# Kernel optimization log

Hardware: AMD Instinct MI355X
Metric: run time of the kernel (lower is better)

## Reference

```python
import jax, jax.numpy as jnp
import numpy as np

NUM_EMB = 16384
EMB_DIM = 64
BETA = 0.25  # commitment_cost, legacy=True formulation


def _l2norm(x, axis=-1):
    # matches F.normalize(p=2): x / max(||x||, 1e-12)
    n = jnp.sqrt(jnp.sum(x * x, axis=axis, keepdims=True))
    return x / jnp.maximum(n, 1e-12)


def setup_inputs() -> dict:
    key = jax.random.key(0)
    k_z, k_cb, k_w, k_b = jax.random.split(key, 4)
    z = jax.random.normal(k_z, (16, 1024, EMB_DIM), dtype=jnp.float32)
    # frozen codebook: N(0, d^{-0.5})
    codebook = jax.random.normal(k_cb, (NUM_EMB, EMB_DIM), dtype=jnp.float32) * (EMB_DIM ** -0.5)
    # Linear(d, d) default init: U(-1/sqrt(d), 1/sqrt(d))
    lim = 1.0 / np.sqrt(EMB_DIM)
    proj_w = jax.random.uniform(k_w, (EMB_DIM, EMB_DIM), dtype=jnp.float32, minval=-lim, maxval=lim)
    proj_b = jax.random.uniform(k_b, (EMB_DIM,), dtype=jnp.float32, minval=-lim, maxval=lim)
    scale = jnp.float32(10.0)  # l2_norm_scale
    return {"z": z, "codebook": codebook, "proj_w": proj_w, "proj_b": proj_b, "scale": scale}


def reference(z, codebook, proj_w, proj_b, scale):
    B, T, d = z.shape
    zf = z.reshape(-1, d)                                   # [BT, d]
    quant_codebook = codebook @ proj_w.T + proj_b           # [N, d]
    zn = _l2norm(zf)
    cn = _l2norm(quant_codebook)
    distances = -jnp.einsum('bd,nd->bn', zn, cn) * scale    # [BT, N]
    idx = jnp.argmin(distances, axis=1)                     # [BT]
    quantized = quant_codebook[idx].reshape(z.shape)        # [B, T, d]
    sg = jax.lax.stop_gradient
    commitment_loss = jnp.mean((sg(quantized) - z) ** 2)
    codebook_loss = jnp.mean((quantized - sg(z)) ** 2)
    vq_loss = commitment_loss + BETA * codebook_loss        # legacy=True
    quantized_st = z + sg(quantized - z)                    # straight-through
    return quantized_st, vq_loss, idx.reshape(B, T)
```

## Files before the change

### kernel.cpp

```cpp
#include <hip/hip_runtime.h>
#include <hip/hip_bf16.h>


#define NCODES 16384
#define NTOK   16384
#define DIM    64
#define MARGIN_MFMA 8e-3f
#define CAP    16

typedef __attribute__((ext_vector_type(8))) short bf16x8;
typedef __attribute__((ext_vector_type(4))) float f32x4;
#define GLOBAL_AS __attribute__((address_space(1)))
#define LDS_AS    __attribute__((address_space(3)))

__device__ float  g_qcb[NCODES * DIM];
__device__ short  g_cnb[NCODES * DIM];
__device__ short  g_znb[NTOK * DIM];
__device__ unsigned g_topu[NTOK];
__device__ int    g_candcnt[NTOK];
__device__ int    g_cand[NTOK * CAP];
__device__ int    g_wl[NTOK];
__device__ int    g_wln;
__device__ float  g_partial[512];

__device__ __forceinline__ float wave_sum64(float v) {
#pragma unroll
  for (int o = 32; o > 0; o >>= 1) v += __shfl_xor(v, o, 64);
  return v;
}
__device__ __forceinline__ short f2bf(float f) {
  __hip_bfloat16 h = __float2bfloat16(f);
  return *reinterpret_cast<short*>(&h);
}
__device__ __forceinline__ float bf2f(short s) {
  __hip_bfloat16 h = *reinterpret_cast<__hip_bfloat16*>(&s);
  return __bfloat162float(h);
}
__device__ __forceinline__ void split8(const float* v, bf16x8& hi, bf16x8& lo) {
#pragma unroll
  for (int i = 0; i < 8; ++i) {
    float f = v[i];
    short h = f2bf(f);
    hi[i] = h;
    lo[i] = f2bf(f - bf2f(h));
  }
}

__global__ __launch_bounds__(256) void k_prep(const float* __restrict__ cb,
                                              const float* __restrict__ pw,
                                              const float* __restrict__ pb,
                                              const float* __restrict__ z) {
  int tid = threadIdx.x;
  int wave = tid >> 6, lane = tid & 63, quad = lane >> 4, col = lane & 15;
  if (blockIdx.x < 256) {
    int rowBase = blockIdx.x * 64 + wave * 16;
    const float* cr = cb + (size_t)(rowBase + col) * 64 + quad * 8;
    bf16x8 ah0, al0, ah1, al1;
    split8(cr, ah0, al0);
    split8(cr + 32, ah1, al1);
    float vals[4][4];
    float nr[4] = {0.f, 0.f, 0.f, 0.f};
    const f32x4 fz = {0.f, 0.f, 0.f, 0.f};
#pragma unroll
    for (int nt = 0; nt < 4; ++nt) {
      int j = col + 16 * nt;
      const float* wr = pw + (size_t)j * 64 + quad * 8;
      bf16x8 bh0, bl0, bh1, bl1;
      split8(wr, bh0, bl0);
      split8(wr + 32, bh1, bl1);
      f32x4 d = __builtin_amdgcn_mfma_f32_16x16x32_bf16(ah0, bh0, fz, 0, 0, 0);
      d = __builtin_amdgcn_mfma_f32_16x16x32_bf16(ah1, bh1, d, 0, 0, 0);
      d = __builtin_amdgcn_mfma_f32_16x16x32_bf16(ah0, bl0, d, 0, 0, 0);
      d = __builtin_amdgcn_mfma_f32_16x16x32_bf16(ah1, bl1, d, 0, 0, 0);
      d = __builtin_amdgcn_mfma_f32_16x16x32_bf16(al0, bh0, d, 0, 0, 0);
      d = __builtin_amdgcn_mfma_f32_16x16x32_bf16(al1, bh1, d, 0, 0, 0);
      float bj = pb[j];
#pragma unroll
      for (int r = 0; r < 4; ++r) {
        float v = d[r] + bj;
        vals[nt][r] = v;
        nr[r] = fmaf(v, v, nr[r]);
      }
    }
#pragma unroll
    for (int r = 0; r < 4; ++r) {
      float v = nr[r];
      v += __shfl_xor(v, 1, 64);
      v += __shfl_xor(v, 2, 64);
      v += __shfl_xor(v, 4, 64);
      v += __shfl_xor(v, 8, 64);
      nr[r] = 1.0f / fmaxf(sqrtf(v), 1e-12f);
    }
#pragma unroll
    for (int nt = 0; nt < 4; ++nt)
#pragma unroll
      for (int r = 0; r < 4; ++r) {
        int row = rowBase + quad * 4 + r;
        int j = col + 16 * nt;
        g_qcb[(size_t)row * 64 + j] = vals[nt][r];
        g_cnb[(size_t)row * 64 + j] = f2bf(vals[nt][r] * nr[r]);
      }
  } else {
    int zb = blockIdx.x - 256;
    int gid = zb * 256 + tid;
    if (gid < NTOK) { g_topu[gid] = 0u; g_candcnt[gid] = 0; }
    if (gid == 0) g_wln = 0;
    int base = zb * 64;
    for (int r = 0; r < 16; ++r) {
      int row = base + wave * 16 + r;
      float v = z[(size_t)row * 64 + lane];
      float tot = wave_sum64(v * v);
      g_znb[(size_t)row * 64 + lane] = f2bf(v / fmaxf(sqrtf(tot), 1e-12f));
    }
  }
}

__global__ __launch_bounds__(256) void k_mfma1() {
  __shared__ __align__(16) short smB[2][8192];
  int tid = threadIdx.x;
  int wave = tid >> 6, lane = tid & 63;
  int quad = lane >> 4, col = lane & 15;
  int tokBlock = blockIdx.x >> 3, split = blockIdx.x & 7;
  int tokBase = tokBlock * 128 + wave * 32;

  const short* za = g_znb + (size_t)(tokBase + col) * 64 + quad * 8;
  bf16x8 A0[2], A1[2];
#pragma unroll
  for (int f = 0; f < 2; ++f) {
    A0[f] = *(const bf16x8*)(za + f * 16 * 64);
    A1[f] = *(const bf16x8*)(za + f * 16 * 64 + 32);
  }
  float m[2][4];
#pragma unroll
  for (int f = 0; f < 2; ++f)
#pragma unroll
    for (int r = 0; r < 4; ++r) m[f][r] = -3.0e38f;

  const char* gsplit = (const char*)(g_cnb + (size_t)split * 2048 * 64);
  int x = col & 7;
  int s0off = ((quad ^ x) << 3);
  int s1off = (((4 | quad) ^ x) << 3);
  int goff[4];
#pragma unroll
  for (int i = 0; i < 4; ++i) {
    int cidx = wave * 256 + i * 64 + lane;
    int row = cidx >> 3, sw = cidx & 7;
    goff[i] = row * 128 + ((sw ^ (row & 7)) << 4);
  }

#pragma unroll
  for (int i = 0; i < 4; ++i)
    __builtin_amdgcn_global_load_lds((const GLOBAL_AS void*)(gsplit + goff[i]),
                                     (LDS_AS void*)(&smB[0][wave * 2048 + i * 512]), 16, 0, 0);
  __syncthreads();

  int p = 0;
  for (int s = 0; s < 16; ++s) {
    if (s < 15) {
      const char* gb = gsplit + (size_t)(s + 1) * 16384;
#pragma unroll
      for (int i = 0; i < 4; ++i)
        __builtin_amdgcn_global_load_lds((const GLOBAL_AS void*)(gb + goff[i]),
                                         (LDS_AS void*)(&smB[p ^ 1][wave * 2048 + i * 512]),
                                         16, 0, 0);
    }
    const short* bufp = smB[p];
#pragma unroll
    for (int t = 0; t < 8; ++t) {
      const short* lb = bufp + (t * 16 + col) * 64;
      bf16x8 b0 = *(const bf16x8*)(lb + s0off);
      bf16x8 b1 = *(const bf16x8*)(lb + s1off);
#pragma unroll
      for (int f = 0; f < 2; ++f) {
        f32x4 acc = {0.f, 0.f, 0.f, 0.f};
        acc = __builtin_amdgcn_mfma_f32_16x16x32_bf16(A0[f], b0, acc, 0, 0, 0);
        acc = __builtin_amdgcn_mfma_f32_16x16x32_bf16(A1[f], b1, acc, 0, 0, 0);
#pragma unroll
        for (int r = 0; r < 4; ++r) m[f][r] = fmaxf(m[f][r], acc[r]);
      }
    }
    __syncthreads();
    p ^= 1;
  }

#pragma unroll
  for (int f = 0; f < 2; ++f)
#pragma unroll
    for (int r = 0; r < 4; ++r) {
      float v = m[f][r];
      v = fmaxf(v, __shfl_xor(v, 1, 64));
      v = fmaxf(v, __shfl_xor(v, 2, 64));
      v = fmaxf(v, __shfl_xor(v, 4, 64));
      v = fmaxf(v, __shfl_xor(v, 8, 64));
      if (col == 0) {
        unsigned b = __float_as_uint(v);
        unsigned e = (b & 0x80000000u) ? ~b : (b | 0x80000000u);
        atomicMax(&g_topu[tokBase + f * 16 + quad * 4 + r], e);
      }
    }
}

__global__ __launch_bounds__(256) void k_mfma2() {
  __shared__ __align__(16) short smB[2][8192];
  int tid = threadIdx.x;
  int wave = tid >> 6, lane = tid & 63;
  int quad = lane >> 4, col = lane & 15;
  int tokBlock = blockIdx.x >> 3, split = blockIdx.x & 7;
  int tokBase = tokBlock * 128 + wave * 32;

  const short* za = g_znb + (size_t)(tokBase + col) * 64 + quad * 8;
  bf16x8 A0[2], A1[2];
#pragma unroll
  for (int f = 0; f < 2; ++f) {
    A0[f] = *(const bf16x8*)(za + f * 16 * 64);
    A1[f] = *(const bf16x8*)(za + f * 16 * 64 + 32);
  }
  float th[2][4];
#pragma unroll
  for (int f = 0; f < 2; ++f)
#pragma unroll
    for (int r = 0; r < 4; ++r) {
      unsigned u = g_topu[tokBase + f * 16 + quad * 4 + r];
      unsigned b = (u & 0x80000000u) ? (u & 0x7FFFFFFFu) : ~u;
      th[f][r] = __uint_as_float(b) - MARGIN_MFMA;
    }

  const char* gsplit = (const char*)(g_cnb + (size_t)split * 2048 * 64);
  int x = col & 7;
  int s0off = ((quad ^ x) << 3);
  int s1off = (((4 | quad) ^ x) << 3);
  int goff[4];
#pragma unroll
  for (int i = 0; i < 4; ++i) {
    int cidx = wave * 256 + i * 64 + lane;
    int row = cidx >> 3, sw = cidx & 7;
    goff[i] = row * 128 + ((sw ^ (row & 7)) << 4);
  }

#pragma unroll
  for (int i = 0; i < 4; ++i)
    __builtin_amdgcn_global_load_lds((const GLOBAL_AS void*)(gsplit + goff[i]),
                                     (LDS_AS void*)(&smB[0][wave * 2048 + i * 512]), 16, 0, 0);
  __syncthreads();

  int codeB = split * 2048 + col;
  int p = 0;
  for (int s = 0; s < 16; ++s) {
    if (s < 15) {
      const char* gb = gsplit + (size_t)(s + 1) * 16384;
#pragma unroll
      for (int i = 0; i < 4; ++i)
        __builtin_amdgcn_global_load_lds((const GLOBAL_AS void*)(gb + goff[i]),
                                         (LDS_AS void*)(&smB[p ^ 1][wave * 2048 + i * 512]),
                                         16, 0, 0);
    }
    const short* bufp = smB[p];
#pragma unroll
    for (int t = 0; t < 8; ++t) {
      const short* lb = bufp + (t * 16 + col) * 64;
      bf16x8 b0 = *(const bf16x8*)(lb + s0off);
      bf16x8 b1 = *(const bf16x8*)(lb + s1off);
      int code = codeB + s * 128 + t * 16;
#pragma unroll
      for (int f = 0; f < 2; ++f) {
        f32x4 acc = {0.f, 0.f, 0.f, 0.f};
        acc = __builtin_amdgcn_mfma_f32_16x16x32_bf16(A0[f], b0, acc, 0, 0, 0);
        acc = __builtin_amdgcn_mfma_f32_16x16x32_bf16(A1[f], b1, acc, 0, 0, 0);
        float dmax = fmaxf(fmaxf(acc[0] - th[f][0], acc[1] - th[f][1]),
                           fmaxf(acc[2] - th[f][2], acc[3] - th[f][3]));
        if (dmax >= 0.f) {
#pragma unroll
          for (int r = 0; r < 4; ++r) {
            if (acc[r] >= th[f][r]) {
              int tok = tokBase + f * 16 + quad * 4 + r;
              int pos = atomicAdd(&g_candcnt[tok], 1);
              if (pos < CAP) g_cand[tok * CAP + pos] = code;
            }
          }
        }
      }
    }
    __syncthreads();
    p ^= 1;
  }
}

__global__ __launch_bounds__(256) void k_scan() {
  __shared__ int flags[256];
  __shared__ int sbase;
  int tid = threadIdx.x;
  int tok = blockIdx.x * 256 + tid;
  int flag = (g_candcnt[tok] >= 2) ? 1 : 0;
  flags[tid] = flag;
  __syncthreads();
  if (tid == 0) {
    int run = 0;
    for (int i = 0; i < 256; ++i) {
      int f = flags[i];
      flags[i] = run;
      run += f;
    }
    sbase = atomicAdd(&g_wln, run);
  }
  __syncthreads();
  if (flag) g_wl[sbase + flags[tid]] = tok;
}

__global__ __launch_bounds__(256) void k_arb(const float* __restrict__ z,
                                             const float* __restrict__ cb,
                                             const float* __restrict__ pw,
                                             const float* __restrict__ pb) {
  __shared__ double WT[64 * 65];
  __shared__ float cbl[4][64];
  int tid = threadIdx.x;
  int wave = tid >> 6, lane = tid & 63;
  for (int e = tid; e < 4096; e += 256) {
    int j = e >> 6, k = e & 63;
    WT[k * 65 + j] = (double)pw[e];
  }
  __syncthreads();

  int wln = g_wln;
  double bj = (double)pb[lane];
  int gwave = blockIdx.x * 4 + wave;

  for (int e = gwave; e < wln; e += 1024) {
    int tok = g_wl[e];
    int cnt = g_candcnt[tok];
    double zj = (double)z[(size_t)tok * 64 + lane];
    double best = -1.0e300;
    int bi = 0x7FFFFFFF;
    int lim = (cnt <= CAP) ? cnt : 0;
    for (int c = 0; c < lim; ++c) {
      int code = g_cand[tok * CAP + c];
      cbl[wave][lane] = cb[(size_t)code * 64 + lane];
      double s0 = 0.0, s1 = 0.0, s2 = 0.0, s3 = 0.0;
#pragma unroll
      for (int kk = 0; kk < 16; ++kk) {
        s0 = fma(WT[kk * 65 + lane], (double)cbl[wave][kk], s0);
        s1 = fma(WT[(kk + 16) * 65 + lane], (double)cbl[wave][kk + 16], s1);
        s2 = fma(WT[(kk + 32) * 65 + lane], (double)cbl[wave][kk + 32], s2);
        s3 = fma(WT[(kk + 48) * 65 + lane], (double)cbl[wave][kk + 48], s3);
      }
      double qc = ((s0 + s1) + (s2 + s3)) + bj;
      double s = zj * qc, n2 = qc * qc;
#pragma unroll
      for (int o = 32; o > 0; o >>= 1) {
        s += __shfl_xor(s, o, 64);
        n2 += __shfl_xor(n2, o, 64);
      }
      double key = s / fmax(sqrt(n2), 1e-12);
      if (key > best || (key == best && code < bi)) { best = key; bi = code; }
    }
    if (cnt > CAP) {
      for (int code = 0; code < NCODES; ++code) {
        cbl[wave][lane] = cb[(size_t)code * 64 + lane];
        double s0 = 0.0, s1 = 0.0, s2 = 0.0, s3 = 0.0;
#pragma unroll
        for (int kk = 0; kk < 16; ++kk) {
          s0 = fma(WT[kk * 65 + lane], (double)cbl[wave][kk], s0);
          s1 = fma(WT[(kk + 16) * 65 + lane], (double)cbl[wave][kk + 16], s1);
          s2 = fma(WT[(kk + 32) * 65 + lane], (double)cbl[wave][kk + 32], s2);
          s3 = fma(WT[(kk + 48) * 65 + lane], (double)cbl[wave][kk + 48], s3);
        }
        double qc = ((s0 + s1) + (s2 + s3)) + bj;
        double s = zj * qc, n2 = qc * qc;
#pragma unroll
        for (int o = 32; o > 0; o >>= 1) {
          s += __shfl_xor(s, o, 64);
          n2 += __shfl_xor(n2, o, 64);
        }
        double key = s / fmax(sqrt(n2), 1e-12);
        if (key > best || (key == best && code < bi)) { best = key; bi = code; }
      }
    }
    if (lane == 0) g_cand[tok * CAP] = bi;
  }
}

__global__ __launch_bounds__(256) void k_out(const float* __restrict__ z,
                                             float* __restrict__ out0,
                                             float* __restrict__ out2) {
  __shared__ float ws[4];
  int tid = threadIdx.x;
  int wave = tid >> 6, lane = tid & 63;
  int base = blockIdx.x * 32;
  float lsum = 0.f;
  for (int r = 0; r < 8; ++r) {
    int tok = base + wave * 8 + r;
    int idx = g_cand[tok * CAP];
    float q = g_qcb[(size_t)idx * 64 + lane];
    float zv = z[(size_t)tok * 64 + lane];
    float d = q - zv;
    out0[(size_t)tok * 64 + lane] = zv + d;
    lsum = fmaf(d, d, lsum);
    if (lane == 0) out2[tok] = (float)idx;
  }
  float tot = wave_sum64(lsum);
  if (lane == 0) ws[wave] = tot;
  __syncthreads();
  if (tid == 0) g_partial[blockIdx.x] = ((ws[0] + ws[1]) + (ws[2] + ws[3]));
}

__global__ void k_loss(float* __restrict__ out1) {
  int lane = threadIdx.x;
  float s = 0.f;
#pragma unroll
  for (int i = 0; i < 8; ++i) s += g_partial[lane + 64 * i];
  s = wave_sum64(s);
  if (lane == 0) out1[0] = 1.25f * s / 1048576.0f;
}

extern "C" void kernel_launch(void* const* d_in, const int* in_sizes, int n_in,
                              void* d_out, int out_size, void* d_ws, size_t ws_size,
                              hipStream_t stream) {
  const float* z = (const float*)d_in[0];
  const float* cb = (const float*)d_in[1];
  const float* pw = (const float*)d_in[2];
  const float* pb = (const float*)d_in[3];

  float* out0 = (float*)d_out;
  float* out1 = out0 + (size_t)NTOK * DIM;
  float* out2 = out1 + 1;

  hipLaunchKernelGGL(k_prep, dim3(512), dim3(256), 0, stream, cb, pw, pb, z);
  hipLaunchKernelGGL(k_mfma1, dim3(1024), dim3(256), 0, stream);
  hipLaunchKernelGGL(k_mfma2, dim3(1024), dim3(256), 0, stream);
  hipLaunchKernelGGL(k_scan, dim3(64), dim3(256), 0, stream);
  hipLaunchKernelGGL(k_arb, dim3(256), dim3(256), 0, stream, z, cb, pw, pb);
  hipLaunchKernelGGL(k_out, dim3(512), dim3(256), 0, stream, z, out0, out2);
  hipLaunchKernelGGL(k_loss, dim3(1), dim3(64), 0, stream, out1);
}
```

Measured before the change: 205.3 us.

## Drop LDS staging of codebook; load B fragments directly from global, 64 tokens per wave

Both MFMA passes stop staging codebook tiles in shared memory with async global-to-LDS copies and barriers. Each wave now reads its B fragments straight from global memory, relying on L1/L2 since all four waves read the same codes. Each wave also covers 64 tokens instead of 32, so each B load feeds twice as many MFMAs and the grid is halved. This trades the LDS traffic and barriers for more global load latency with no explicit prefetch, plus higher register pressure.

```diff
diff --git a/kernel.cpp b/kernel.cpp
--- a/kernel.cpp
+++ b/kernel.cpp
@@ -10,8 +10,6 @@
 
 typedef __attribute__((ext_vector_type(8))) short bf16x8;
 typedef __attribute__((ext_vector_type(4))) float f32x4;
-#define GLOBAL_AS __attribute__((address_space(1)))
-#define LDS_AS    __attribute__((address_space(3)))
 
 __device__ float  g_qcb[NCODES * DIM];
 __device__ short  g_cnb[NCODES * DIM];
@@ -116,75 +114,44 @@
 }
 
 __global__ __launch_bounds__(256) void k_mfma1() {
-  __shared__ __align__(16) short smB[2][8192];
   int tid = threadIdx.x;
   int wave = tid >> 6, lane = tid & 63;
   int quad = lane >> 4, col = lane & 15;
-  int tokBlock = blockIdx.x >> 3, split = blockIdx.x & 7;
-  int tokBase = tokBlock * 128 + wave * 32;
+  int tokGroup = blockIdx.x >> 3, split = blockIdx.x & 7;
+  int tokBase = tokGroup * 256 + wave * 64;
 
   const short* za = g_znb + (size_t)(tokBase + col) * 64 + quad * 8;
-  bf16x8 A0[2], A1[2];
-#pragma unroll
-  for (int f = 0; f < 2; ++f) {
+  bf16x8 A0[4], A1[4];
+#pragma unroll
+  for (int f = 0; f < 4; ++f) {
     A0[f] = *(const bf16x8*)(za + f * 16 * 64);
     A1[f] = *(const bf16x8*)(za + f * 16 * 64 + 32);
   }
-  float m[2][4];
-#pragma unroll
-  for (int f = 0; f < 2; ++f)
+  float m[4][4];
+#pragma unroll
+  for (int f = 0; f < 4; ++f)
 #pragma unroll
     for (int r = 0; r < 4; ++r) m[f][r] = -3.0e38f;
 
-  const char* gsplit = (const char*)(g_cnb + (size_t)split * 2048 * 64);
-  int x = col & 7;
-  int s0off = ((quad ^ x) << 3);
-  int s1off = (((4 | quad) ^ x) << 3);
-  int goff[4];
-#pragma unroll
-  for (int i = 0; i < 4; ++i) {
-    int cidx = wave * 256 + i * 64 + lane;
-    int row = cidx >> 3, sw = cidx & 7;
-    goff[i] = row * 128 + ((sw ^ (row & 7)) << 4);
-  }
-
-#pragma unroll
-  for (int i = 0; i < 4; ++i)
-    __builtin_amdgcn_global_load_lds((const GLOBAL_AS void*)(gsplit + goff[i]),
-                                     (LDS_AS void*)(&smB[0][wave * 2048 + i * 512]), 16, 0, 0);
-  __syncthreads();
-
-  int p = 0;
-  for (int s = 0; s < 16; ++s) {
-    if (s < 15) {
-      const char* gb = gsplit + (size_t)(s + 1) * 16384;
-#pragma unroll
-      for (int i = 0; i < 4; ++i)
-        __builtin_amdgcn_global_load_lds((const GLOBAL_AS void*)(gb + goff[i]),
-                                         (LDS_AS void*)(&smB[p ^ 1][wave * 2048 + i * 512]),
-                                         16, 0, 0);
-    }
-    const short* bufp = smB[p];
-#pragma unroll
-    for (int t = 0; t < 8; ++t) {
-      const short* lb = bufp + (t * 16 + col) * 64;
-      bf16x8 b0 = *(const bf16x8*)(lb + s0off);
-      bf16x8 b1 = *(const bf16x8*)(lb + s1off);
-#pragma unroll
-      for (int f = 0; f < 2; ++f) {
-        f32x4 acc = {0.f, 0.f, 0.f, 0.f};
-        acc = __builtin_amdgcn_mfma_f32_16x16x32_bf16(A0[f], b0, acc, 0, 0, 0);
-        acc = __builtin_amdgcn_mfma_f32_16x16x32_bf16(A1[f], b1, acc, 0, 0, 0);
-#pragma unroll
-        for (int r = 0; r < 4; ++r) m[f][r] = fmaxf(m[f][r], acc[r]);
-      }
-    }
-    __syncthreads();
-    p ^= 1;
-  }
-
-#pragma unroll
-  for (int f = 0; f < 2; ++f)
+  const short* bp = g_cnb + ((size_t)split * 2048 + col) * 64 + quad * 8;
+
+#pragma unroll 4
+  for (int t = 0; t < 128; ++t) {
+    const short* pt = bp + t * 1024;
+    bf16x8 b0 = *(const bf16x8*)(pt);
+    bf16x8 b1 = *(const bf16x8*)(pt + 32);
+#pragma unroll
+    for (int f = 0; f < 4; ++f) {
+      f32x4 acc = {0.f, 0.f, 0.f, 0.f};
+      acc = __builtin_amdgcn_mfma_f32_16x16x32_bf16(A0[f], b0, acc, 0, 0, 0);
+      acc = __builtin_amdgcn_mfma_f32_16x16x32_bf16(A1[f], b1, acc, 0, 0, 0);
+#pragma unroll
+      for (int r = 0; r < 4; ++r) m[f][r] = fmaxf(m[f][r], acc[r]);
+    }
+  }
+
+#pragma unroll
+  for (int f = 0; f < 4; ++f)
 #pragma unroll
     for (int r = 0; r < 4; ++r) {
       float v = m[f][r];
@@ -201,23 +168,22 @@
 }
 
 __global__ __launch_bounds__(256) void k_mfma2() {
-  __shared__ __align__(16) short smB[2][8192];
   int tid = threadIdx.x;
   int wave = tid >> 6, lane = tid & 63;
   int quad = lane >> 4, col = lane & 15;
-  int tokBlock = blockIdx.x >> 3, split = blockIdx.x & 7;
-  int tokBase = tokBlock * 128 + wave * 32;
+  int tokGroup = blockIdx.x >> 3, split = blockIdx.x & 7;
+  int tokBase = tokGroup * 256 + wave * 64;
 
   const short* za = g_znb + (size_t)(tokBase + col) * 64 + quad * 8;
-  bf16x8 A0[2], A1[2];
-#pragma unroll
-  for (int f = 0; f < 2; ++f) {
+  bf16x8 A0[4], A1[4];
+#pragma unroll
+  for (int f = 0; f < 4; ++f) {
     A0[f] = *(const bf16x8*)(za + f * 16 * 64);
     A1[f] = *(const bf16x8*)(za + f * 16 * 64 + 32);
   }
-  float th[2][4];
-#pragma unroll
-  for (int f = 0; f < 2; ++f)
+  float th[4][4];
+#pragma unroll
+  for (int f = 0; f < 4; ++f)
 #pragma unroll
     for (int r = 0; r < 4; ++r) {
       unsigned u = g_topu[tokBase + f * 16 + quad * 4 + r];
@@ -225,63 +191,33 @@
       th[f][r] = __uint_as_float(b) - MARGIN_MFMA;
     }
 
-  const char* gsplit = (const char*)(g_cnb + (size_t)split * 2048 * 64);
-  int x = col & 7;
-  int s0off = ((quad ^ x) << 3);
-  int s1off = (((4 | quad) ^ x) << 3);
-  int goff[4];
-#pragma unroll
-  for (int i = 0; i < 4; ++i) {
-    int cidx = wave * 256 + i * 64 + lane;
-    int row = cidx >> 3, sw = cidx & 7;
-    goff[i] = row * 128 + ((sw ^ (row & 7)) << 4);
-  }
-
-#pragma unroll
-  for (int i = 0; i < 4; ++i)
-    __builtin_amdgcn_global_load_lds((const GLOBAL_AS void*)(gsplit + goff[i]),
-                                     (LDS_AS void*)(&smB[0][wave * 2048 + i * 512]), 16, 0, 0);
-  __syncthreads();
-
+  const short* bp = g_cnb + ((size_t)split * 2048 + col) * 64 + quad * 8;
   int codeB = split * 2048 + col;
-  int p = 0;
-  for (int s = 0; s < 16; ++s) {
-    if (s < 15) {
-      const char* gb = gsplit + (size_t)(s + 1) * 16384;
-#pragma unroll
-      for (int i = 0; i < 4; ++i)
-        __builtin_amdgcn_global_load_lds((const GLOBAL_AS void*)(gb + goff[i]),
-                                         (LDS_AS void*)(&smB[p ^ 1][wave * 2048 + i * 512]),
-                                         16, 0, 0);
-    }
-    const short* bufp = smB[p];
-#pragma unroll
-    for (int t = 0; t < 8; ++t) {
-      const short* lb = bufp + (t * 16 + col) * 64;
-      bf16x8 b0 = *(const bf16x8*)(lb + s0off);
-      bf16x8 b1 = *(const bf16x8*)(lb + s1off);
-      int code = codeB + s * 128 + t * 16;
-#pragma unroll
-      for (int f = 0; f < 2; ++f) {
-        f32x4 acc = {0.f, 0.f, 0.f, 0.f};
-        acc = __builtin_amdgcn_mfma_f32_16x16x32_bf16(A0[f], b0, acc, 0, 0, 0);
-        acc = __builtin_amdgcn_mfma_f32_16x16x32_bf16(A1[f], b1, acc, 0, 0, 0);
-        float dmax = fmaxf(fmaxf(acc[0] - th[f][0], acc[1] - th[f][1]),
-                           fmaxf(acc[2] - th[f][2], acc[3] - th[f][3]));
-        if (dmax >= 0.f) {
-#pragma unroll
-          for (int r = 0; r < 4; ++r) {
-            if (acc[r] >= th[f][r]) {
-              int tok = tokBase + f * 16 + quad * 4 + r;
-              int pos = atomicAdd(&g_candcnt[tok], 1);
-              if (pos < CAP) g_cand[tok * CAP + pos] = code;
-            }
+
+#pragma unroll 4
+  for (int t = 0; t < 128; ++t) {
+    const short* pt = bp + t * 1024;
+    bf16x8 b0 = *(const bf16x8*)(pt);
+    bf16x8 b1 = *(const bf16x8*)(pt + 32);
+    int code = codeB + t * 16;
+#pragma unroll
+    for (int f = 0; f < 4; ++f) {
+      f32x4 acc = {0.f, 0.f, 0.f, 0.f};
+      acc = __builtin_amdgcn_mfma_f32_16x16x32_bf16(A0[f], b0, acc, 0, 0, 0);
+      acc = __builtin_amdgcn_mfma_f32_16x16x32_bf16(A1[f], b1, acc, 0, 0, 0);
+      float dmax = fmaxf(fmaxf(acc[0] - th[f][0], acc[1] - th[f][1]),
+                         fmaxf(acc[2] - th[f][2], acc[3] - th[f][3]));
+      if (dmax >= 0.f) {
+#pragma unroll
+        for (int r = 0; r < 4; ++r) {
+          if (acc[r] >= th[f][r]) {
+            int tok = tokBase + f * 16 + quad * 4 + r;
+            int pos = atomicAdd(&g_candcnt[tok], 1);
+            if (pos < CAP) g_cand[tok * CAP + pos] = code;
           }
         }
       }
     }
-    __syncthreads();
-    p ^= 1;
   }
 }
 
@@ -424,8 +360,8 @@
   float* out2 = out1 + 1;
 
   hipLaunchKernelGGL(k_prep, dim3(512), dim3(256), 0, stream, cb, pw, pb, z);
-  hipLaunchKernelGGL(k_mfma1, dim3(1024), dim3(256), 0, stream);
-  hipLaunchKernelGGL(k_mfma2, dim3(1024), dim3(256), 0, stream);
+  hipLaunchKernelGGL(k_mfma1, dim3(512), dim3(256), 0, stream);
+  hipLaunchKernelGGL(k_mfma2, dim3(512), dim3(256), 0, stream);
   hipLaunchKernelGGL(k_scan, dim3(64), dim3(256), 0, stream);
   hipLaunchKernelGGL(k_arb, dim3(256), dim3(256), 0, stream, z, cb, pw, pb);
   hipLaunchKernelGGL(k_out, dim3(512), dim3(256), 0, stream, z, out0, out2);
```

Result: slower. 268.9 us (+31.0%).
